# Kernel optimization log

Hardware: AMD Instinct MI355X
Metric: run time of the kernel (lower is better)

Reference implementation:

```python
import jax, jax.numpy as jnp
import numpy as np

B, S, D, H, EXP = 4, 2048, 768, 8, 4
HD = D // H  # head dim = 96
EPS = 1e-5


def layer_norm(x, g, b):
    mu = jnp.mean(x, axis=-1, keepdims=True)
    var = jnp.mean(jnp.square(x - mu), axis=-1, keepdims=True)
    return (x - mu) * jax.lax.rsqrt(var + EPS) * g + b


def setup_inputs() -> dict:
    key = jax.random.key(0)
    ks = jax.random.split(key, 16)
    s = 0.02
    f32 = jnp.float32
    x = jax.random.normal(ks[0], (B, S, D), f32)
    Wq = jax.random.normal(ks[1], (D, D), f32) * s
    bq = jnp.zeros((D,), f32)
    Wk = jax.random.normal(ks[2], (D, D), f32) * s
    bk = jnp.zeros((D,), f32)
    Wv = jax.random.normal(ks[3], (D, D), f32) * s
    bv = jnp.zeros((D,), f32)
    Wo = jax.random.normal(ks[4], (D, D), f32) * s
    bo = jnp.zeros((D,), f32)
    g1 = jnp.ones((D,), f32)
    be1 = jnp.zeros((D,), f32)
    W1 = jax.random.normal(ks[5], (D, D * EXP), f32) * s
    bf1 = jnp.zeros((D * EXP,), f32)
    W2 = jax.random.normal(ks[6], (D * EXP, D), f32) * s
    bf2 = jnp.zeros((D,), f32)
    g2 = jnp.ones((D,), f32)
    be2 = jnp.zeros((D,), f32)
    return dict(x=x, Wq=Wq, bq=bq, Wk=Wk, bk=bk, Wv=Wv, bv=bv, Wo=Wo, bo=bo,
                g1=g1, be1=be1, W1=W1, bf1=bf1, W2=W2, bf2=bf2, g2=g2, be2=be2)


def reference(x, Wq, bq, Wk, bk, Wv, bv, Wo, bo, g1, be1, W1, bf1, W2, bf2, g2, be2):
    scale = HD ** (-0.5)
    # multi-head attention (manual QK^T softmax V)
    q = (x @ Wq + bq).reshape(B, S, H, HD).transpose(0, 2, 1, 3)  # b H s c
    k = (x @ Wk + bk).reshape(B, S, H, HD).transpose(0, 2, 1, 3)
    v = (x @ Wv + bv).reshape(B, S, H, HD).transpose(0, 2, 1, 3)
    scores = jnp.einsum('bhqc,bhkc->bhqk', q, k) * scale
    attn = jax.nn.softmax(scores, axis=-1)
    o = jnp.einsum('bhqk,bhkc->bhqc', attn, v)
    o = o.transpose(0, 2, 1, 3).reshape(B, S, D)
    attn_out = o @ Wo + bo
    # residual + LN
    x1 = layer_norm(attn_out + x, g1, be1)
    # feed-forward with GELU
    h = jax.nn.gelu(x1 @ W1 + bf1)
    ffn_out = h @ W2 + bf2
    # residual + LN
    return layer_norm(ffn_out + x1, g2, be2)
```

## Files before the change

kernel.cpp:

```cpp
#include <hip/hip_runtime.h>
#include <hip/hip_bf16.h>
#include <math.h>
#include <stdint.h>

#define B_    4
#define S_    2048
#define D_    768
#define H_    8
#define HD_   96
#define EXPD_ 3072
#define MSZ   8192

#define QSCALE 0.14724439f
#define M0_    12.0f

typedef __bf16 bf16;
typedef __bf16 bf16x4 __attribute__((ext_vector_type(4)));
typedef __bf16 bf16x8 __attribute__((ext_vector_type(8)));
typedef float  f32x4  __attribute__((ext_vector_type(4)));

typedef __attribute__((address_space(1))) const uint32_t gu32;
typedef __attribute__((address_space(3))) uint32_t lu32;

__device__ __forceinline__ void async_copy16(const void* g, void* l) {
    __builtin_amdgcn_global_load_lds((gu32*)g, (lu32*)l, 16, 0, 0);
}

__device__ __forceinline__ float gelu_f(float x) {
    float x3 = x * x * x;
    return 0.5f * x * (1.0f + tanhf(0.7978845608028654f * (x + 0.044715f * x3)));
}

__device__ __forceinline__ bool sniff_f32(const void* p) {
    const bf16* pb = (const bf16*)p;
    float v = (float)pb[2 * (threadIdx.x & 63)];
    bool big = !(fabsf(v) < 1000.0f);
    return __any(big) != 0;
}

__device__ __forceinline__ float dynld(const void* p, size_t i, bool f32in) {
    return f32in ? ((const float*)p)[i] : (float)((const bf16*)p)[i];
}

__global__ __launch_bounds__(256) void cast_kernel(
    const void* __restrict__ src, bf16* __restrict__ dst)
{
    const bool f32in = sniff_f32(src);
    size_t i = ((size_t)blockIdx.x * 256 + threadIdx.x) * 8;
    if (f32in) {
        f32x4 a = *(const f32x4*)((const float*)src + i);
        f32x4 b = *(const f32x4*)((const float*)src + i + 4);
        bf16x8 r;
#pragma unroll
        for (int e = 0; e < 4; ++e) { r[e] = (bf16)a[e]; r[e + 4] = (bf16)b[e]; }
        *(bf16x8*)(dst + i) = r;
    } else {
        *(bf16x8*)(dst + i) = *(const bf16x8*)((const bf16*)src + i);
    }
}

#define MODE_QKV  0
#define MODE_RES  1
#define MODE_GELU 2

template<int MODE, bool ADYN, bool RESDYN, int BN>
__global__ __launch_bounds__(256) void gemm2_kernel(
    const void* __restrict__ A, const bf16* __restrict__ Bt,
    const void* __restrict__ b0, const void* __restrict__ b1, const void* __restrict__ b2,
    const void* __restrict__ res, bf16* __restrict__ out,
    int M, int N, int K, int ldb, int boff, const void* __restrict__ sniffp)
{
    constexpr int WN = BN / 2;
    constexpr int NJ = WN / 16;
    __shared__ __align__(16) bf16 As[128 * 32];
    __shared__ __align__(16) bf16 Bs[BN * 32];

    const bool f32in = sniff_f32(sniffp);
    const int tid  = threadIdx.x;
    const int w    = tid >> 6;
    const int lane = tid & 63;
    const int quad = lane >> 4;
    const int l16  = lane & 15;
    const int wr   = w >> 1, wc = w & 1;
    const int m0   = blockIdx.x * 128;
    const int n0   = blockIdx.y * BN;

    const int rsub = lane >> 2;
    const int cb8  = (lane & 3) * 8;

    f32x4 acc[4][NJ];
#pragma unroll
    for (int i = 0; i < 4; ++i)
#pragma unroll
        for (int j = 0; j < NJ; ++j) acc[i][j] = (f32x4){0.f, 0.f, 0.f, 0.f};

    const bf16*  Abf = (const bf16*)A;
    const float* Af  = (const float*)A;

    for (int k0 = 0; k0 < K; k0 += 32) {
        __syncthreads();
        if (ADYN && f32in) {
#pragma unroll
            for (int a = 0; a < 2; ++a) {
                int row = w * 32 + a * 16 + rsub;
                const float* sp = Af + (size_t)(m0 + row) * K + k0 + cb8;
                f32x4 u0 = *(const f32x4*)sp;
                f32x4 u1 = *(const f32x4*)(sp + 4);
                bf16x8 v;
#pragma unroll
                for (int e = 0; e < 4; ++e) { v[e] = (bf16)u0[e]; v[e + 4] = (bf16)u1[e]; }
                *(bf16x8*)(&As[(size_t)(w * 32 + a * 16) * 32 + lane * 8]) = v;
            }
        } else {
#pragma unroll
            for (int a = 0; a < 2; ++a) {
                int row = w * 32 + a * 16 + rsub;
                async_copy16(Abf + (size_t)(m0 + row) * K + k0 + cb8,
                             &As[(w * 32 + a * 16) * 32]);
            }
        }
#pragma unroll
        for (int a = 0; a < BN / 64; ++a) {
            int row = w * (BN / 4) + a * 16 + rsub;
            async_copy16(Bt + (size_t)(n0 + row) * ldb + k0 + cb8,
                         &Bs[(w * (BN / 4) + a * 16) * 32]);
        }
        __syncthreads();

        bf16x8 af[4], bfv[NJ];
#pragma unroll
        for (int i = 0; i < 4; ++i)
            af[i]  = *(const bf16x8*)(&As[(wr * 64 + i * 16 + l16) * 32 + quad * 8]);
#pragma unroll
        for (int j = 0; j < NJ; ++j)
            bfv[j] = *(const bf16x8*)(&Bs[(wc * WN + j * 16 + l16) * 32 + quad * 8]);
#pragma unroll
        for (int i = 0; i < 4; ++i)
#pragma unroll
            for (int j = 0; j < NJ; ++j)
                acc[i][j] = __builtin_amdgcn_mfma_f32_16x16x32_bf16(af[i], bfv[j], acc[i][j], 0, 0, 0);
    }

#pragma unroll
    for (int j = 0; j < NJ; ++j) {
        int n = n0 + wc * WN + j * 16 + l16;
        float bval;
        int which = 0, n2 = n;
        if constexpr (MODE == MODE_QKV) {
            which = n / D_;
            n2 = n - which * D_;
            const void* bp = which == 0 ? b0 : (which == 1 ? b1 : b2);
            bval = dynld(bp, n2, f32in);
        } else {
            bval = boff >= 0 ? dynld(b0, boff + n, f32in) : 0.f;
        }
#pragma unroll
        for (int i = 0; i < 4; ++i) {
#pragma unroll
            for (int r = 0; r < 4; ++r) {
                int m = m0 + wr * 64 + i * 16 + quad * 4 + r;
                float v = acc[i][j][r] + bval;
                if constexpr (MODE == MODE_QKV) {
                    int b  = m >> 11;
                    int ss = m & (S_ - 1);
                    int h  = n2 / HD_;
                    int hd = n2 - h * HD_;
                    int bh = b * H_ + h;
                    if (which == 0) v *= QSCALE;
                    size_t dst;
                    if (which < 2)
                        dst = (size_t)which * (MSZ * D_) + ((size_t)bh * S_ + ss) * HD_ + hd;
                    else
                        dst = (size_t)2 * (MSZ * D_) + ((size_t)bh * HD_ + hd) * S_ + ss;
                    out[dst] = (bf16)v;
                } else if constexpr (MODE == MODE_RES) {
                    size_t ri = (size_t)m * N + n;
                    float rv = RESDYN ? dynld(res, ri, f32in) : (float)((const bf16*)res)[ri];
                    out[ri] = (bf16)(v + rv);
                } else {
                    out[(size_t)m * N + n] = (bf16)gelu_f(v);
                }
            }
        }
    }
}

__global__ __launch_bounds__(512, 6) void flash_kernel(
    const bf16* __restrict__ Q, const bf16* __restrict__ Kk,
    const bf16* __restrict__ Vt_g, bf16* __restrict__ ctx)
{
    __shared__ __align__(16) bf16 Ks[64][104];
    __shared__ __align__(16) bf16 Vs[96][72];
    __shared__ __align__(16) bf16 Ps[8][16][72];

    const int tid  = threadIdx.x;
    const int w    = tid >> 6;
    const int lane = tid & 63;
    const int quad = lane >> 4;
    const int l16  = lane & 15;
    const int bh   = blockIdx.y;
    const size_t base = (size_t)bh * S_ * HD_;
    const int q0   = blockIdx.x * 128 + w * 16;

    bf16x8 qf[3];
#pragma unroll
    for (int ch = 0; ch < 3; ++ch)
        qf[ch] = *(const bf16x8*)(Q + base + (size_t)(q0 + l16) * HD_ + ch * 32 + quad * 8);

    f32x4 oacc[6];
#pragma unroll
    for (int c = 0; c < 6; ++c) oacc[c] = (f32x4){0.f, 0.f, 0.f, 0.f};
    float lsum[4] = {0.f, 0.f, 0.f, 0.f};

    const int kvi  = tid & 255;
    const int ch2  = tid >> 8;
    const int krow = kvi >> 2, kc8 = (kvi & 3) * 8 + ch2 * 32;
    const int vrow = (kvi >> 3) + ch2 * 32, vcb = (kvi & 7) * 8;
    const int krow2 = tid >> 2, kc82 = (tid & 3) * 8 + 64;
    const int vrow2 = (tid >> 3) + 64, vcb2 = (tid & 7) * 8;

    for (int kv0 = 0; kv0 < S_; kv0 += 64) {
        __syncthreads();
        *(bf16x8*)(&Ks[krow][kc8]) =
            *(const bf16x8*)(Kk + base + (size_t)(kv0 + krow) * HD_ + kc8);
        *(bf16x8*)(&Vs[vrow][vcb]) =
            *(const bf16x8*)(Vt_g + base + (size_t)vrow * S_ + kv0 + vcb);
        if (tid < 256) {
            *(bf16x8*)(&Ks[krow2][kc82]) =
                *(const bf16x8*)(Kk + base + (size_t)(kv0 + krow2) * HD_ + kc82);
            *(bf16x8*)(&Vs[vrow2][vcb2]) =
                *(const bf16x8*)(Vt_g + base + (size_t)vrow2 * S_ + kv0 + vcb2);
        }
        __syncthreads();

        f32x4 sacc[4];
#pragma unroll
        for (int t = 0; t < 4; ++t) {
            sacc[t] = (f32x4){0.f, 0.f, 0.f, 0.f};
#pragma unroll
            for (int ch = 0; ch < 3; ++ch) {
                bf16x8 kf = *(const bf16x8*)(&Ks[t * 16 + l16][ch * 32 + quad * 8]);
                sacc[t] = __builtin_amdgcn_mfma_f32_16x16x32_bf16(qf[ch], kf, sacc[t], 0, 0, 0);
            }
        }

#pragma unroll
        for (int r = 0; r < 4; ++r) {
            int qr = quad * 4 + r;
            float p0 = exp2f(sacc[0][r] - M0_);
            float p1 = exp2f(sacc[1][r] - M0_);
            float p2 = exp2f(sacc[2][r] - M0_);
            float p3 = exp2f(sacc[3][r] - M0_);
            lsum[r] += (p0 + p1) + (p2 + p3);
            Ps[w][qr][l16]      = (bf16)p0;
            Ps[w][qr][16 + l16] = (bf16)p1;
            Ps[w][qr][32 + l16] = (bf16)p2;
            Ps[w][qr][48 + l16] = (bf16)p3;
        }

        bf16x8 pf0 = *(const bf16x8*)(&Ps[w][l16][quad * 8]);
        bf16x8 pf1 = *(const bf16x8*)(&Ps[w][l16][32 + quad * 8]);
#pragma unroll
        for (int c = 0; c < 6; ++c) {
            bf16x8 vf0 = *(const bf16x8*)(&Vs[c * 16 + l16][quad * 8]);
            bf16x8 vf1 = *(const bf16x8*)(&Vs[c * 16 + l16][32 + quad * 8]);
            oacc[c] = __builtin_amdgcn_mfma_f32_16x16x32_bf16(pf0, vf0, oacc[c], 0, 0, 0);
            oacc[c] = __builtin_amdgcn_mfma_f32_16x16x32_bf16(pf1, vf1, oacc[c], 0, 0, 0);
        }
    }

#pragma unroll
    for (int r = 0; r < 4; ++r)
#pragma unroll
        for (int off = 1; off < 16; off <<= 1)
            lsum[r] += __shfl_xor(lsum[r], off);

    const int b = bh >> 3, h = bh & 7;
#pragma unroll
    for (int r = 0; r < 4; ++r) {
        float inv = 1.0f / lsum[r];
        int srow = q0 + quad * 4 + r;
        size_t rowbase = ((size_t)b * S_ + srow) * D_ + h * HD_;
#pragma unroll
        for (int c = 0; c < 6; ++c)
            ctx[rowbase + c * 16 + l16] = (bf16)(oacc[c][r] * inv);
    }
}

template<bool OUTDYN>
__global__ __launch_bounds__(256) void ln_kernel(
    const bf16* __restrict__ in, const void* __restrict__ g, const void* __restrict__ be,
    void* __restrict__ out, const void* __restrict__ sniffp)
{
    const bool f32in = sniff_f32(sniffp);
    const int w = threadIdx.x >> 6, lane = threadIdx.x & 63;
    const int row = blockIdx.x * 4 + w;
    const size_t rbase = (size_t)row * D_ + lane * 12;

    float v[12];
#pragma unroll
    for (int j = 0; j < 3; ++j) {
        bf16x4 t = *(const bf16x4*)(in + rbase + j * 4);
#pragma unroll
        for (int e = 0; e < 4; ++e) v[j * 4 + e] = (float)t[e];
    }
    float sum = 0.f;
#pragma unroll
    for (int j = 0; j < 12; ++j) sum += v[j];
#pragma unroll
    for (int off = 1; off < 64; off <<= 1) sum += __shfl_xor(sum, off);
    float mu = sum * (1.0f / D_);
    float sq = 0.f;
#pragma unroll
    for (int j = 0; j < 12; ++j) { v[j] -= mu; sq += v[j] * v[j]; }
#pragma unroll
    for (int off = 1; off < 64; off <<= 1) sq += __shfl_xor(sq, off);
    float rstd = rsqrtf(sq * (1.0f / D_) + 1e-5f);

    if (OUTDYN && f32in) {
        float* op = (float*)out + rbase;
#pragma unroll
        for (int j = 0; j < 3; ++j) {
            f32x4 t;
#pragma unroll
            for (int e = 0; e < 4; ++e) {
                int c = lane * 12 + j * 4 + e;
                t[e] = v[j * 4 + e] * rstd * dynld(g, c, true) + dynld(be, c, true);
            }
            *(f32x4*)(op + j * 4) = t;
        }
    } else {
        bf16* op = (bf16*)out + rbase;
#pragma unroll
        for (int j = 0; j < 3; ++j) {
            bf16x4 t;
#pragma unroll
            for (int e = 0; e < 4; ++e) {
                int c = lane * 12 + j * 4 + e;
                t[e] = (bf16)(v[j * 4 + e] * rstd * dynld(g, c, f32in) + dynld(be, c, f32in));
            }
            *(bf16x4*)(op + j * 4) = t;
        }
    }
}

__device__ __forceinline__ void transpose_tile(
    const void* __restrict__ src, bf16* __restrict__ dst, int R, int C,
    int r0, int c0, bool f32in)
{
    __shared__ bf16 t[64][65];
    const int tx = threadIdx.x & 63, ty = threadIdx.x >> 6;
#pragma unroll
    for (int i = 0; i < 16; ++i) {
        int rr = ty + i * 4;
        t[rr][tx] = (bf16)dynld(src, (size_t)(r0 + rr) * C + c0 + tx, f32in);
    }
    __syncthreads();
#pragma unroll
    for (int i = 0; i < 16; ++i) {
        int cc = ty + i * 4;
        dst[(size_t)(c0 + cc) * R + r0 + tx] = t[tx][cc];
    }
}

__global__ __launch_bounds__(256) void transpose_qkv_kernel(
    const void* __restrict__ s0, const void* __restrict__ s1, const void* __restrict__ s2,
    bf16* __restrict__ dst)
{
    const void* src = blockIdx.z == 0 ? s0 : (blockIdx.z == 1 ? s1 : s2);
    const bool f32in = sniff_f32(src);
    transpose_tile(src, dst + (size_t)blockIdx.z * D_ * D_, D_, D_,
                   blockIdx.y * 64, blockIdx.x * 64, f32in);
}

__global__ __launch_bounds__(256) void transpose_mlp_kernel(
    const void* __restrict__ s0, const void* __restrict__ s1, const void* __restrict__ s2,
    bf16* __restrict__ dst)
{
    int z = blockIdx.z;
    const void* src = z == 0 ? s0 : (z == 1 ? s1 : s2);
    int R = z == 2 ? EXPD_ : D_;
    int C = z == 1 ? EXPD_ : D_;
    size_t off = z == 0 ? 0 : (z == 1 ? (size_t)D_ * D_ : (size_t)D_ * D_ + (size_t)D_ * EXPD_);
    int r0 = blockIdx.y * 64, c0 = blockIdx.x * 64;
    if (r0 >= R || c0 >= C) return;
    const bool f32in = sniff_f32(src);
    transpose_tile(src, dst + off, R, C, r0, c0, f32in);
}

extern "C" void kernel_launch(void* const* d_in, const int* in_sizes, int n_in,
                              void* d_out, int out_size, void* d_ws, size_t ws_size,
                              hipStream_t stream)
{
    (void)in_sizes; (void)n_in; (void)out_size;
    const void* x   = d_in[0];
    const void* Wq  = d_in[1];
    const void* bq  = d_in[2];
    const void* Wk  = d_in[3];
    const void* bk  = d_in[4];
    const void* Wv  = d_in[5];
    const void* bv  = d_in[6];
    const void* Wo  = d_in[7];
    const void* bo  = d_in[8];
    const void* g1  = d_in[9];
    const void* be1 = d_in[10];
    const void* W1  = d_in[11];
    const void* bf1 = d_in[12];
    const void* W2  = d_in[13];
    const void* bf2 = d_in[14];
    const void* g2  = d_in[15];
    const void* be2 = d_in[16];

    const size_t REG = (size_t)MSZ * D_ * 2;
    char* p = (char*)d_ws;
    bf16* R0 = (bf16*)p;
    bf16* R1 = (bf16*)(p + REG);
    bf16* R2 = (bf16*)(p + 2 * REG);
    bf16* R3 = (bf16*)(p + 3 * REG);
    bf16* R4 = (bf16*)(p + 4 * REG);
    const bool nsplit = ws_size >= 5 * REG;

    bf16* qkvT = (bf16*)d_out;
    bf16* ctx  = (bf16*)d_out;
    dim3 blk(256);

    if (nsplit) cast_kernel<<<dim3(MSZ * D_ / (256 * 8)), blk, 0, stream>>>(x, R4);

    transpose_qkv_kernel<<<dim3(12, 12, 3), blk, 0, stream>>>(Wq, Wk, Wv, qkvT);

    if (nsplit)
        gemm2_kernel<MODE_QKV, false, false, 128><<<dim3(MSZ / 128, 2304 / 128), blk, 0, stream>>>(
            R4, qkvT, bq, bk, bv, nullptr, R0, MSZ, 2304, D_, D_, 0, Wq);
    else
        gemm2_kernel<MODE_QKV, true, false, 128><<<dim3(MSZ / 128, 2304 / 128), blk, 0, stream>>>(
            x, qkvT, bq, bk, bv, nullptr, R0, MSZ, 2304, D_, D_, 0, Wq);

    flash_kernel<<<dim3(S_ / 128, B_ * H_), dim3(512), 0, stream>>>(R0, R1, R2, ctx);

    bf16* WoT = R1;
    bf16* W1T = WoT + (size_t)D_ * D_;
    bf16* W2T = W1T + (size_t)D_ * EXPD_;
    transpose_mlp_kernel<<<dim3(48, 48, 3), blk, 0, stream>>>(Wo, W1, W2, WoT);

    if (nsplit)
        gemm2_kernel<MODE_RES, false, false, 64><<<dim3(MSZ / 128, D_ / 64), blk, 0, stream>>>(
            ctx, WoT, bo, nullptr, nullptr, R4, R3, MSZ, D_, D_, D_, 0, Wq);
    else
        gemm2_kernel<MODE_RES, false, true, 64><<<dim3(MSZ / 128, D_ / 64), blk, 0, stream>>>(
            ctx, WoT, bo, nullptr, nullptr, x, R3, MSZ, D_, D_, D_, 0, Wq);

    bf16* x1b = R0;
    ln_kernel<false><<<dim3(MSZ / 4), blk, 0, stream>>>(R3, g1, be1, x1b, Wq);

    bf16* y2b;
    if (nsplit) {
        bf16* hb = R2;
        y2b = R4;
        gemm2_kernel<MODE_GELU, false, false, 128><<<dim3(MSZ / 128, 12), blk, 0, stream>>>(
            x1b, W1T, bf1, nullptr, nullptr, nullptr, hb, MSZ, 1536, D_, D_, 0, Wq);
        gemm2_kernel<MODE_RES, false, false, 64><<<dim3(MSZ / 128, D_ / 64), blk, 0, stream>>>(
            hb, W2T, bf2, nullptr, nullptr, x1b, y2b, MSZ, D_, 1536, EXPD_, 0, Wq);
        gemm2_kernel<MODE_GELU, false, false, 128><<<dim3(MSZ / 128, 12), blk, 0, stream>>>(
            x1b, W1T + (size_t)1536 * D_, bf1, nullptr, nullptr, nullptr, hb, MSZ, 1536, D_, D_, 1536, Wq);
        gemm2_kernel<MODE_RES, false, false, 64><<<dim3(MSZ / 128, D_ / 64), blk, 0, stream>>>(
            hb, W2T + 1536, nullptr, nullptr, nullptr, y2b, y2b, MSZ, D_, 1536, EXPD_, -1, Wq);
    } else {
        bf16* hb = R3;
        y2b = R2;
        const int CH = 2048;
        for (int c0 = 0; c0 < MSZ; c0 += CH) {
            const bf16* x1c = x1b + (size_t)c0 * D_;
            gemm2_kernel<MODE_GELU, false, false, 128><<<dim3(CH / 128, EXPD_ / 128), blk, 0, stream>>>(
                x1c, W1T, bf1, nullptr, nullptr, nullptr, hb, CH, EXPD_, D_, D_, 0, Wq);
            gemm2_kernel<MODE_RES, false, false, 64><<<dim3(CH / 128, D_ / 64), blk, 0, stream>>>(
                hb, W2T, bf2, nullptr, nullptr, x1c, y2b + (size_t)c0 * D_, CH, D_, EXPD_, EXPD_, 0, Wq);
        }
    }

    ln_kernel<true><<<dim3(MSZ / 4), blk, 0, stream>>>(y2b, g2, be2, d_out, Wq);
}
```

Baseline: 506.3 us.

## Stage GEMM epilogue through LDS for vector stores, add full-FFN tier, reorder flash grid

The GEMM epilogue for residual and GELU modes now writes accumulators into shared memory per wave and then reads them back as 8-wide rows, so global stores and residual loads are 16-byte vectorized instead of scalar. A new workspace tier, used when the workspace is large enough, runs the FFN as one full-width W1 GEMM and one K=3072 W2 GEMM instead of two halves, cutting launches and the read-modify-write of the output. The flash kernel grid is swapped so consecutive blocks cover different heads, and the MLP transpose launches a flat 1D grid with no empty blocks. The extra barrier and LDS round trip add some epilogue latency, and the new FFN tier only runs if the workspace is large enough.

New measurement: 471.2 us. 6.9% less time.

```diff
diff --git a/kernel.cpp b/kernel.cpp
--- a/kernel.cpp
+++ b/kernel.cpp
@@ -72,8 +72,9 @@
 {
     constexpr int WN = BN / 2;
     constexpr int NJ = WN / 16;
-    __shared__ __align__(16) bf16 As[128 * 32];
-    __shared__ __align__(16) bf16 Bs[BN * 32];
+    __shared__ __align__(16) bf16 Sh[8192];
+    bf16* As = Sh;
+    bf16* Bs = Sh + 4096;
 
     const bool f32in = sniff_f32(sniffp);
     const int tid  = threadIdx.x;
@@ -141,26 +142,20 @@
                 acc[i][j] = __builtin_amdgcn_mfma_f32_16x16x32_bf16(af[i], bfv[j], acc[i][j], 0, 0, 0);
     }
 
-#pragma unroll
-    for (int j = 0; j < NJ; ++j) {
-        int n = n0 + wc * WN + j * 16 + l16;
-        float bval;
-        int which = 0, n2 = n;
-        if constexpr (MODE == MODE_QKV) {
-            which = n / D_;
-            n2 = n - which * D_;
+    if constexpr (MODE == MODE_QKV) {
+#pragma unroll
+        for (int j = 0; j < NJ; ++j) {
+            int n = n0 + wc * WN + j * 16 + l16;
+            int which = n / D_;
+            int n2 = n - which * D_;
             const void* bp = which == 0 ? b0 : (which == 1 ? b1 : b2);
-            bval = dynld(bp, n2, f32in);
-        } else {
-            bval = boff >= 0 ? dynld(b0, boff + n, f32in) : 0.f;
-        }
-#pragma unroll
-        for (int i = 0; i < 4; ++i) {
-#pragma unroll
-            for (int r = 0; r < 4; ++r) {
-                int m = m0 + wr * 64 + i * 16 + quad * 4 + r;
-                float v = acc[i][j][r] + bval;
-                if constexpr (MODE == MODE_QKV) {
+            float bval = dynld(bp, n2, f32in);
+#pragma unroll
+            for (int i = 0; i < 4; ++i) {
+#pragma unroll
+                for (int r = 0; r < 4; ++r) {
+                    int m = m0 + wr * 64 + i * 16 + quad * 4 + r;
+                    float v = acc[i][j][r] + bval;
                     int b  = m >> 11;
                     int ss = m & (S_ - 1);
                     int h  = n2 / HD_;
@@ -173,12 +168,53 @@
                     else
                         dst = (size_t)2 * (MSZ * D_) + ((size_t)bh * HD_ + hd) * S_ + ss;
                     out[dst] = (bf16)v;
-                } else if constexpr (MODE == MODE_RES) {
-                    size_t ri = (size_t)m * N + n;
-                    float rv = RESDYN ? dynld(res, ri, f32in) : (float)((const bf16*)res)[ri];
-                    out[ri] = (bf16)(v + rv);
+                }
+            }
+        }
+    } else {
+        __syncthreads();
+        bf16* Cw = Sh + w * 2048;
+        for (int jp = 0; jp < NJ / 2; ++jp) {
+#pragma unroll
+            for (int j2 = 0; j2 < 2; ++j2) {
+                int j = jp * 2 + j2;
+                int n = n0 + wc * WN + j * 16 + l16;
+                float bval = boff >= 0 ? dynld(b0, boff + n, f32in) : 0.f;
+#pragma unroll
+                for (int i = 0; i < 4; ++i)
+#pragma unroll
+                    for (int r = 0; r < 4; ++r) {
+                        float v = acc[i][j][r] + bval;
+                        if constexpr (MODE == MODE_GELU) v = gelu_f(v);
+                        Cw[(i * 16 + quad * 4 + r) * 32 + j2 * 16 + l16] = (bf16)v;
+                    }
+            }
+#pragma unroll
+            for (int pass = 0; pass < 4; ++pass) {
+                int row = pass * 16 + (lane >> 2);
+                int cc  = (lane & 3) * 8;
+                bf16x8 cv = *(const bf16x8*)&Cw[row * 32 + cc];
+                int m = m0 + wr * 64 + row;
+                int n = n0 + wc * WN + jp * 32 + cc;
+                size_t off = (size_t)m * N + n;
+                if constexpr (MODE == MODE_RES) {
+                    bf16x8 o;
+                    if (RESDYN && f32in) {
+                        f32x4 r0 = *(const f32x4*)((const float*)res + off);
+                        f32x4 r1 = *(const f32x4*)((const float*)res + off + 4);
+#pragma unroll
+                        for (int e = 0; e < 4; ++e) {
+                            o[e]     = (bf16)((float)cv[e] + r0[e]);
+                            o[e + 4] = (bf16)((float)cv[e + 4] + r1[e]);
+                        }
+                    } else {
+                        bf16x8 rv = *(const bf16x8*)((const bf16*)res + off);
+#pragma unroll
+                        for (int e = 0; e < 8; ++e) o[e] = (bf16)((float)cv[e] + (float)rv[e]);
+                    }
+                    *(bf16x8*)&out[off] = o;
                 } else {
-                    out[(size_t)m * N + n] = (bf16)gelu_f(v);
+                    *(bf16x8*)&out[off] = cv;
                 }
             }
         }
@@ -198,9 +234,9 @@
     const int lane = tid & 63;
     const int quad = lane >> 4;
     const int l16  = lane & 15;
-    const int bh   = blockIdx.y;
+    const int bh   = blockIdx.x;
     const size_t base = (size_t)bh * S_ * HD_;
-    const int q0   = blockIdx.x * 128 + w * 16;
+    const int q0   = blockIdx.y * 128 + w * 16;
 
     bf16x8 qf[3];
 #pragma unroll
@@ -377,15 +413,18 @@
     const void* __restrict__ s0, const void* __restrict__ s1, const void* __restrict__ s2,
     bf16* __restrict__ dst)
 {
-    int z = blockIdx.z;
-    const void* src = z == 0 ? s0 : (z == 1 ? s1 : s2);
-    int R = z == 2 ? EXPD_ : D_;
-    int C = z == 1 ? EXPD_ : D_;
-    size_t off = z == 0 ? 0 : (z == 1 ? (size_t)D_ * D_ : (size_t)D_ * D_ + (size_t)D_ * EXPD_);
-    int r0 = blockIdx.y * 64, c0 = blockIdx.x * 64;
-    if (r0 >= R || c0 >= C) return;
+    int id = blockIdx.x;
+    const void* src;
+    int R, C, r, c;
+    size_t off;
+    if (id < 144)      { src = s0; R = D_;    C = D_;    off = 0;
+                         r = id / 12;          c = id % 12; }
+    else if (id < 720) { src = s1; R = D_;    C = EXPD_; off = (size_t)D_ * D_;
+                         int i = id - 144;     r = i / 48; c = i % 48; }
+    else               { src = s2; R = EXPD_; C = D_;    off = (size_t)D_ * D_ + (size_t)D_ * EXPD_;
+                         int i = id - 720;     r = i / 12; c = i % 12; }
     const bool f32in = sniff_f32(src);
-    transpose_tile(src, dst + off, R, C, r0, c0, f32in);
+    transpose_tile(src, dst + off, R, C, r * 64, c * 64, f32in);
 }
 
 extern "C" void kernel_launch(void* const* d_in, const int* in_sizes, int n_in,
@@ -418,33 +457,37 @@
     bf16* R2 = (bf16*)(p + 2 * REG);
     bf16* R3 = (bf16*)(p + 3 * REG);
     bf16* R4 = (bf16*)(p + 4 * REG);
-    const bool nsplit = ws_size >= 5 * REG;
+
+    int tier = 0;
+    if      (ws_size >= 9 * REG) tier = 3;
+    else if (ws_size >= 5 * REG) tier = 1;
+    bf16* xb = tier == 3 ? (bf16*)(p + 8 * REG) : R4;
 
     bf16* qkvT = (bf16*)d_out;
     bf16* ctx  = (bf16*)d_out;
     dim3 blk(256);
 
-    if (nsplit) cast_kernel<<<dim3(MSZ * D_ / (256 * 8)), blk, 0, stream>>>(x, R4);
+    if (tier >= 1) cast_kernel<<<dim3(MSZ * D_ / (256 * 8)), blk, 0, stream>>>(x, xb);
 
     transpose_qkv_kernel<<<dim3(12, 12, 3), blk, 0, stream>>>(Wq, Wk, Wv, qkvT);
 
-    if (nsplit)
+    if (tier >= 1)
         gemm2_kernel<MODE_QKV, false, false, 128><<<dim3(MSZ / 128, 2304 / 128), blk, 0, stream>>>(
-            R4, qkvT, bq, bk, bv, nullptr, R0, MSZ, 2304, D_, D_, 0, Wq);
+            xb, qkvT, bq, bk, bv, nullptr, R0, MSZ, 2304, D_, D_, 0, Wq);
     else
         gemm2_kernel<MODE_QKV, true, false, 128><<<dim3(MSZ / 128, 2304 / 128), blk, 0, stream>>>(
             x, qkvT, bq, bk, bv, nullptr, R0, MSZ, 2304, D_, D_, 0, Wq);
 
-    flash_kernel<<<dim3(S_ / 128, B_ * H_), dim3(512), 0, stream>>>(R0, R1, R2, ctx);
+    flash_kernel<<<dim3(B_ * H_, S_ / 128), dim3(512), 0, stream>>>(R0, R1, R2, ctx);
 
     bf16* WoT = R1;
     bf16* W1T = WoT + (size_t)D_ * D_;
     bf16* W2T = W1T + (size_t)D_ * EXPD_;
-    transpose_mlp_kernel<<<dim3(48, 48, 3), blk, 0, stream>>>(Wo, W1, W2, WoT);
-
-    if (nsplit)
+    transpose_mlp_kernel<<<dim3(1296), blk, 0, stream>>>(Wo, W1, W2, WoT);
+
+    if (tier >= 1)
         gemm2_kernel<MODE_RES, false, false, 64><<<dim3(MSZ / 128, D_ / 64), blk, 0, stream>>>(
-            ctx, WoT, bo, nullptr, nullptr, R4, R3, MSZ, D_, D_, D_, 0, Wq);
+            ctx, WoT, bo, nullptr, nullptr, xb, R3, MSZ, D_, D_, D_, 0, Wq);
     else
         gemm2_kernel<MODE_RES, false, true, 64><<<dim3(MSZ / 128, D_ / 64), blk, 0, stream>>>(
             ctx, WoT, bo, nullptr, nullptr, x, R3, MSZ, D_, D_, D_, 0, Wq);
@@ -453,7 +496,14 @@
     ln_kernel<false><<<dim3(MSZ / 4), blk, 0, stream>>>(R3, g1, be1, x1b, Wq);
 
     bf16* y2b;
-    if (nsplit) {
+    if (tier == 3) {
+        bf16* hb = R4;
+        y2b = R3;
+        gemm2_kernel<MODE_GELU, false, false, 128><<<dim3(MSZ / 128, EXPD_ / 128), blk, 0, stream>>>(
+            x1b, W1T, bf1, nullptr, nullptr, nullptr, hb, MSZ, EXPD_, D_, D_, 0, Wq);
+        gemm2_kernel<MODE_RES, false, false, 64><<<dim3(MSZ / 128, D_ / 64), blk, 0, stream>>>(
+            hb, W2T, bf2, nullptr, nullptr, x1b, y2b, MSZ, D_, EXPD_, EXPD_, 0, Wq);
+    } else if (tier == 1) {
         bf16* hb = R2;
         y2b = R4;
         gemm2_kernel<MODE_GELU, false, false, 128><<<dim3(MSZ / 128, 12), blk, 0, stream>>>(
```
